# Performance work log

Hardware: AMD Instinct MI355X
Metric: run time of the kernel (lower is better)

The kernel has to match this reference:

```python
import jax, jax.numpy as jnp
import numpy as np

DIM = 512
HEADS = 8
DIM_HEAD = 64
INNER = HEADS * DIM_HEAD
SCALE = DIM_HEAD ** -0.5


def setup_inputs() -> dict:
    key = jax.random.key(0)
    ks = jax.random.split(key, 6)
    b, n = 2, 2048
    x = jax.random.normal(ks[0], (b, n, DIM), dtype=jnp.float32)
    # torch Linear(dim, 3*inner, bias=False): store as [in, out] for x @ W
    w_qkv = jax.random.normal(ks[1], (DIM, 3 * INNER), dtype=jnp.float32) * (DIM ** -0.5)
    # Conv2d(heads, heads, 1, bias=False) weights squeezed to [out_h, in_h]
    w_pre = jax.random.normal(ks[2], (HEADS, HEADS), dtype=jnp.float32) * (HEADS ** -0.5)
    w_post = jax.random.normal(ks[3], (HEADS, HEADS), dtype=jnp.float32) * (HEADS ** -0.5)
    w_out = jax.random.normal(ks[4], (INNER, DIM), dtype=jnp.float32) * (INNER ** -0.5)
    b_out = jax.random.normal(ks[5], (DIM,), dtype=jnp.float32) * 0.01
    return {"x": x, "w_qkv": w_qkv, "w_pre": w_pre, "w_post": w_post,
            "w_out": w_out, "b_out": b_out}


def reference(x, w_qkv, w_pre, w_post, w_out, b_out):
    b, n, _ = x.shape
    qkv = x @ w_qkv  # [b, n, 3*inner]
    q, k, v = jnp.split(qkv, 3, axis=-1)
    # b n (h d) -> b h n d
    split_heads = lambda t: t.reshape(b, n, HEADS, DIM_HEAD).transpose(0, 2, 1, 3)
    q, k, v = split_heads(q), split_heads(k), split_heads(v)
    dots = jnp.einsum('bhid,bhjd->bhij', q, k) * SCALE
    # pre-softmax talking-heads: 1x1 conv over the head axis
    dots = jnp.einsum('gh,bhij->bgij', w_pre, dots)
    attn = jax.nn.softmax(dots, axis=-1)
    # post-softmax talking-heads mix
    attn = jnp.einsum('gh,bhij->bgij', w_post, attn)
    out = jnp.einsum('bhij,bhjd->bhid', attn, v)
    out = out.transpose(0, 2, 1, 3).reshape(b, n, INNER)  # b h n d -> b n (h d)
    return out @ w_out + b_out
```

## Files before the change

kernel.cpp:

```cpp
#include <hip/hip_runtime.h>
#include <hip/hip_bf16.h>

typedef unsigned short ushort_t;
typedef __attribute__((ext_vector_type(8))) short short8;
typedef __attribute__((ext_vector_type(4))) short short4v;
typedef __attribute__((ext_vector_type(4))) float floatx4;

#define MFMA16(a, b, c) __builtin_amdgcn_mfma_f32_16x16x32_bf16(a, b, c, 0, 0, 0)

__device__ __forceinline__ float bf2f(ushort_t u) {
    unsigned int v = ((unsigned int)u) << 16;
    return __int_as_float((int)v);
}
__device__ __forceinline__ ushort_t f2bf(float f) {
    unsigned int x = (unsigned int)__float_as_int(f);
    unsigned int r = (x + 0x7FFFu + ((x >> 16) & 1u)) >> 16;
    return (ushort_t)r;
}
__device__ __forceinline__ floatx4 fma4(float a, floatx4 b, floatx4 c) {
    c[0] = fmaf(a, b[0], c[0]);
    c[1] = fmaf(a, b[1], c[1]);
    c[2] = fmaf(a, b[2], c[2]);
    c[3] = fmaf(a, b[3], c[3]);
    return c;
}

__global__ __launch_bounds__(256) void k_cvt(const floatx4* __restrict__ src,
                                             short4v* __restrict__ dst, int n4) {
    int i = blockIdx.x * 256 + threadIdx.x;
    if (i < n4) {
        floatx4 v = src[i];
        short4v o;
        o[0] = (short)f2bf(v[0]);
        o[1] = (short)f2bf(v[1]);
        o[2] = (short)f2bf(v[2]);
        o[3] = (short)f2bf(v[3]);
        dst[i] = o;
    }
}

__global__ __launch_bounds__(256) void k_transpose_cvt(const float* __restrict__ src,
                                                       ushort_t* __restrict__ dst, int R, int C) {
    __shared__ float t[32][33];
    int tx = threadIdx.x & 31, ty = threadIdx.x >> 5;
    int r0 = blockIdx.y * 32, c0 = blockIdx.x * 32;
    for (int y = ty; y < 32; y += 8) t[y][tx] = src[(r0 + y) * C + c0 + tx];
    __syncthreads();
    for (int y = ty; y < 32; y += 8) dst[(c0 + y) * R + r0 + tx] = f2bf(t[tx][y]);
}

__global__ __launch_bounds__(256) void k_qkv(const ushort_t* __restrict__ x,
                                             const ushort_t* __restrict__ wt,
                                             ushort_t* __restrict__ qs,
                                             ushort_t* __restrict__ ks,
                                             ushort_t* __restrict__ vt) {
    __shared__ __align__(16) ushort_t st[64 * 72];
    const int tid = threadIdx.x, lane = tid & 63, wv = tid >> 6;
    const int col = lane & 15, quad = lane >> 4;
    const int row0 = blockIdx.y * 64 + (wv >> 1) * 32;
    const int c0 = blockIdx.x * 64 + (wv & 1) * 32;
    const int which = blockIdx.x >> 3, hh = blockIdx.x & 7;
    const int brow0 = blockIdx.y * 64;
    const int bb = brow0 >> 11, n0 = brow0 & 2047;
    const int hidx = bb * 8 + hh;
    floatx4 acc[2][2];
#pragma unroll
    for (int i = 0; i < 2; i++)
#pragma unroll
        for (int j = 0; j < 2; j++) acc[i][j] = (floatx4){0.f, 0.f, 0.f, 0.f};
    for (int k0 = 0; k0 < 512; k0 += 32) {
        const int ko = k0 + quad * 8;
        short8 a0 = *(const short8*)&x[(row0 + col) * 512 + ko];
        short8 a1 = *(const short8*)&x[(row0 + 16 + col) * 512 + ko];
        short8 b0 = *(const short8*)&wt[(c0 + col) * 512 + ko];
        short8 b1 = *(const short8*)&wt[(c0 + 16 + col) * 512 + ko];
        acc[0][0] = MFMA16(a0, b0, acc[0][0]);
        acc[0][1] = MFMA16(a0, b1, acc[0][1]);
        acc[1][0] = MFMA16(a1, b0, acc[1][0]);
        acc[1][1] = MFMA16(a1, b1, acc[1][1]);
    }
    const float qscale = (which == 0) ? 0.125f : 1.0f;
#pragma unroll
    for (int i = 0; i < 2; i++)
#pragma unroll
        for (int j = 0; j < 2; j++)
#pragma unroll
            for (int r = 0; r < 4; r++) {
                int il = (wv >> 1) * 32 + i * 16 + quad * 4 + r;
                int cl = (wv & 1) * 32 + j * 16 + col;
                ushort_t hv = f2bf(acc[i][j][r] * qscale);
                if (which == 2) st[cl * 72 + il] = hv;
                else            st[il * 72 + cl] = hv;
            }
    __syncthreads();
    if (which < 2) {
        ushort_t* dst = (which == 0) ? qs : ks;
#pragma unroll
        for (int s = tid; s < 512; s += 256) {
            int rr = s >> 3, dc = (s & 7) * 8;
            *(short8*)&dst[(hidx * 2048 + n0 + rr) * 64 + dc] = *(const short8*)&st[rr * 72 + dc];
        }
    } else {
#pragma unroll
        for (int s = tid; s < 512; s += 256) {
            int d = s >> 3, nc = (s & 7) * 8;
            *(short8*)&vt[(hidx * 64 + d) * 2048 + n0 + nc] = *(const short8*)&st[d * 72 + nc];
        }
    }
}

__global__ __launch_bounds__(512, 2) void k_attn(const ushort_t* __restrict__ qs,
                                                 const ushort_t* __restrict__ ks,
                                                 const ushort_t* __restrict__ vt,
                                                 const float* __restrict__ w_pre,
                                                 const float* __restrict__ w_post,
                                                 const ushort_t* __restrict__ wot,
                                                 const float* __restrict__ bias,
                                                 float* __restrict__ out) {
    __shared__ __align__(16) ushort_t qlds[8 * 16 * 72];
    __shared__ __align__(16) ushort_t A[2][8 * 16 * 136];
    __shared__ __align__(16) ushort_t oline[16 * 520];
    __shared__ __align__(16) float wbuf[128];
    __shared__ float lred[8][8][16];
    __shared__ __align__(16) float linv[8][16];
    const int tid = threadIdx.x, lane = tid & 63, wv = tid >> 6;
    const int col = lane & 15, quad = lane >> 4;
    const int b = blockIdx.y, n0 = blockIdx.x * 16;
    const int e = wv;

    if (tid < 64) wbuf[tid] = w_pre[tid];
    else if (tid < 128) wbuf[tid] = w_post[tid - 64];
    for (int c = tid; c < 1024; c += 512) {
        int hh = c >> 7, rem = c & 127, ii = rem >> 3, dc = (rem & 7) * 8;
        *(short8*)&qlds[(hh * 16 + ii) * 72 + dc] =
            *(const short8*)&qs[((b * 8 + hh) * 2048 + n0 + ii) * 64 + dc];
    }

    short8 kb0[8], kb1[8];
#pragma unroll
    for (int h = 0; h < 8; h++) {
        const ushort_t* kp = &ks[((b * 8 + h) * 2048 + wv * 16 + col) * 64 + quad * 8];
        kb0[h] = *(const short8*)&kp[0];
        kb1[h] = *(const short8*)&kp[32];
    }
    __syncthreads();

    short8 qa0[8], qa1[8];
#pragma unroll
    for (int h = 0; h < 8; h++) {
        const ushort_t* qb = &qlds[(h * 16 + col) * 72 + quad * 8];
        qa0[h] = *(const short8*)&qb[0];
        qa1[h] = *(const short8*)&qb[32];
    }

    floatx4 Lacc[8];
#pragma unroll
    for (int g = 0; g < 8; g++) Lacc[g] = (floatx4){0.f, 0.f, 0.f, 0.f};

    for (int jt = 0; jt < 16; jt++) {
        floatx4 S[8];
#pragma unroll
        for (int h = 0; h < 8; h++) {
            floatx4 a = (floatx4){0.f, 0.f, 0.f, 0.f};
            a = MFMA16(qa0[h], kb0[h], a);
            a = MFMA16(qa1[h], kb1[h], a);
            S[h] = a;
        }
        if (jt < 15) {
            const int jw = (jt + 1) * 128 + wv * 16;
#pragma unroll
            for (int h = 0; h < 8; h++) {
                const ushort_t* kp = &ks[((b * 8 + h) * 2048 + jw + col) * 64 + quad * 8];
                kb0[h] = *(const short8*)&kp[0];
                kb1[h] = *(const short8*)&kp[32];
            }
        }
#pragma unroll
        for (int g = 0; g < 8; g++) {
            floatx4 w0 = *(const floatx4*)&wbuf[g * 8];
            floatx4 w1 = *(const floatx4*)&wbuf[g * 8 + 4];
            floatx4 s4 = (floatx4){0.f, 0.f, 0.f, 0.f};
#pragma unroll
            for (int h = 0; h < 4; h++) s4 = fma4(w0[h], S[h], s4);
#pragma unroll
            for (int h = 0; h < 4; h++) s4 = fma4(w1[h], S[h + 4], s4);
            floatx4 u4;
            u4[0] = __expf(s4[0]);
            u4[1] = __expf(s4[1]);
            u4[2] = __expf(s4[2]);
            u4[3] = __expf(s4[3]);
            Lacc[g] += u4;
        }
    }

#pragma unroll
    for (int g = 0; g < 8; g++)
#pragma unroll
        for (int r = 0; r < 4; r++) {
            float v = Lacc[g][r];
            v += __shfl_xor(v, 1, 64);
            v += __shfl_xor(v, 2, 64);
            v += __shfl_xor(v, 4, 64);
            v += __shfl_xor(v, 8, 64);
            if (col == 0) lred[wv][g][quad * 4 + r] = v;
        }
    __syncthreads();
    if (tid < 128) {
        int g = tid >> 4, ii = tid & 15;
        float l = 0.f;
#pragma unroll
        for (int w2 = 0; w2 < 8; w2++) l += lred[w2][g][ii];
        linv[g][ii] = 1.0f / l;
    }
    __syncthreads();

#pragma unroll
    for (int h = 0; h < 8; h++) {
        const ushort_t* kp = &ks[((b * 8 + h) * 2048 + wv * 16 + col) * 64 + quad * 8];
        kb0[h] = *(const short8*)&kp[0];
        kb1[h] = *(const short8*)&kp[32];
    }
    short8 vbr[16];
#pragma unroll
    for (int k2 = 0; k2 < 4; k2++)
#pragma unroll
        for (int nt = 0; nt < 4; nt++)
            vbr[k2 * 4 + nt] = *(const short8*)&vt[((b * 8 + e) * 64 + nt * 16 + col) * 2048 +
                                                   k2 * 32 + quad * 8];
    floatx4 Oa[4];
#pragma unroll
    for (int nt = 0; nt < 4; nt++) Oa[nt] = (floatx4){0.f, 0.f, 0.f, 0.f};

    int cur = 0;
    for (int jt = 0; jt < 16; jt++) {
        floatx4 S[8];
#pragma unroll
        for (int h = 0; h < 8; h++) {
            const ushort_t* qb = &qlds[(h * 16 + col) * 72 + quad * 8];
            short8 a0 = *(const short8*)&qb[0];
            short8 a1 = *(const short8*)&qb[32];
            floatx4 a = (floatx4){0.f, 0.f, 0.f, 0.f};
            a = MFMA16(a0, kb0[h], a);
            a = MFMA16(a1, kb1[h], a);
            S[h] = a;
        }
        if (jt < 15) {
            const int jw = (jt + 1) * 128 + wv * 16;
#pragma unroll
            for (int h = 0; h < 8; h++) {
                const ushort_t* kp = &ks[((b * 8 + h) * 2048 + jw + col) * 64 + quad * 8];
                kb0[h] = *(const short8*)&kp[0];
                kb1[h] = *(const short8*)&kp[32];
            }
        }
        floatx4 Ug[8];
#pragma unroll
        for (int g = 0; g < 8; g++) {
            floatx4 w0 = *(const floatx4*)&wbuf[g * 8];
            floatx4 w1 = *(const floatx4*)&wbuf[g * 8 + 4];
            floatx4 s4 = (floatx4){0.f, 0.f, 0.f, 0.f};
#pragma unroll
            for (int h = 0; h < 4; h++) s4 = fma4(w0[h], S[h], s4);
#pragma unroll
            for (int h = 0; h < 4; h++) s4 = fma4(w1[h], S[h + 4], s4);
            floatx4 lg = *(const floatx4*)&linv[g][quad * 4];
            floatx4 u4;
            u4[0] = __expf(s4[0]) * lg[0];
            u4[1] = __expf(s4[1]) * lg[1];
            u4[2] = __expf(s4[2]) * lg[2];
            u4[3] = __expf(s4[3]) * lg[3];
            Ug[g] = u4;
        }
        ushort_t* Ac = A[cur];
#pragma unroll
        for (int e2 = 0; e2 < 8; e2++) {
            floatx4 wqa = *(const floatx4*)&wbuf[64 + e2 * 8];
            floatx4 wqb = *(const floatx4*)&wbuf[64 + e2 * 8 + 4];
            floatx4 a4 = (floatx4){0.f, 0.f, 0.f, 0.f};
#pragma unroll
            for (int g = 0; g < 4; g++) a4 = fma4(wqa[g], Ug[g], a4);
#pragma unroll
            for (int g = 0; g < 4; g++) a4 = fma4(wqb[g], Ug[g + 4], a4);
#pragma unroll
            for (int r = 0; r < 4; r++)
                Ac[(e2 * 16 + quad * 4 + r) * 136 + wv * 16 + col] = f2bf(a4[r]);
        }
        asm volatile("s_waitcnt lgkmcnt(0)\n\ts_barrier" ::: "memory");
#pragma unroll
        for (int k2 = 0; k2 < 4; k2++) {
            short8 af = *(const short8*)&Ac[(e * 16 + col) * 136 + k2 * 32 + quad * 8];
#pragma unroll
            for (int nt = 0; nt < 4; nt++) Oa[nt] = MFMA16(af, vbr[k2 * 4 + nt], Oa[nt]);
        }
        if (jt < 15) {
            const int j0 = (jt + 1) * 128;
#pragma unroll
            for (int k2 = 0; k2 < 4; k2++)
#pragma unroll
                for (int nt = 0; nt < 4; nt++)
                    vbr[k2 * 4 + nt] =
                        *(const short8*)&vt[((b * 8 + e) * 64 + nt * 16 + col) * 2048 + j0 +
                                            k2 * 32 + quad * 8];
        }
        cur ^= 1;
    }

#pragma unroll
    for (int nt = 0; nt < 4; nt++)
#pragma unroll
        for (int r = 0; r < 4; r++)
            oline[(quad * 4 + r) * 520 + e * 64 + nt * 16 + col] = f2bf(Oa[nt][r]);
    __syncthreads();
#pragma unroll
    for (int nt = 0; nt < 4; nt++) {
        floatx4 acc = (floatx4){0.f, 0.f, 0.f, 0.f};
        const int c = wv * 64 + nt * 16 + col;
#pragma unroll
        for (int k2 = 0; k2 < 16; k2++) {
            short8 af = *(const short8*)&oline[col * 520 + k2 * 32 + quad * 8];
            short8 bf = *(const short8*)&wot[c * 512 + k2 * 32 + quad * 8];
            acc = MFMA16(af, bf, acc);
        }
        float bz = bias[c];
#pragma unroll
        for (int r = 0; r < 4; r++)
            out[(b * 2048 + n0 + quad * 4 + r) * 512 + c] = acc[r] + bz;
    }
}

extern "C" void kernel_launch(void* const* d_in, const int* in_sizes, int n_in,
                              void* d_out, int out_size, void* d_ws, size_t ws_size,
                              hipStream_t stream) {
    const float* x = (const float*)d_in[0];
    const float* w_qkv = (const float*)d_in[1];
    const float* w_pre = (const float*)d_in[2];
    const float* w_post = (const float*)d_in[3];
    const float* w_out = (const float*)d_in[4];
    const float* b_out = (const float*)d_in[5];
    char* ws = (char*)d_ws;
    ushort_t* qs = (ushort_t*)(ws);
    ushort_t* ks = (ushort_t*)(ws + (4u << 20));
    ushort_t* vt = (ushort_t*)(ws + (8u << 20));
    ushort_t* xb = (ushort_t*)(ws + (12u << 20));
    ushort_t* wt = (ushort_t*)(ws + (16u << 20));
    ushort_t* wot = (ushort_t*)(ws + (16u << 20) + 1572864u);
    float* out = (float*)d_out;

    k_cvt<<<dim3(2048), dim3(256), 0, stream>>>((const floatx4*)x, (short4v*)xb, 524288);
    k_transpose_cvt<<<dim3(48, 16), dim3(256), 0, stream>>>(w_qkv, wt, 512, 1536);
    k_transpose_cvt<<<dim3(16, 16), dim3(256), 0, stream>>>(w_out, wot, 512, 512);
    k_qkv<<<dim3(24, 64), dim3(256), 0, stream>>>(xb, wt, qs, ks, vt);
    k_attn<<<dim3(128, 2), dim3(512), 0, stream>>>(qs, ks, vt, w_pre, w_post, wot, b_out, out);
}
```

Before: 343.5 us.

## Split attention into row-sum, split-KV attention and projection kernels

The fused attention kernel is split into three kernels. A row-sum kernel computes partial softmax denominators over four key chunks. The attention kernel processes half the keys per block and writes fp32 partial outputs. A projection kernel sums the two halves and applies the output projection and bias. The old grid was only 256 blocks, and this split raises it to 512–1024 blocks to fill the GPU's compute units. In exchange it adds global round-trips for the partial sums and partial outputs, plus extra launches, and the A buffer loses its double buffering, which costs an extra barrier per iteration.

```diff
diff --git a/kernel.cpp b/kernel.cpp
--- a/kernel.cpp
+++ b/kernel.cpp
@@ -109,55 +109,39 @@
     }
 }
 
-__global__ __launch_bounds__(512, 2) void k_attn(const ushort_t* __restrict__ qs,
+__global__ __launch_bounds__(256, 4) void k_lsum(const ushort_t* __restrict__ qs,
                                                  const ushort_t* __restrict__ ks,
-                                                 const ushort_t* __restrict__ vt,
                                                  const float* __restrict__ w_pre,
-                                                 const float* __restrict__ w_post,
-                                                 const ushort_t* __restrict__ wot,
-                                                 const float* __restrict__ bias,
-                                                 float* __restrict__ out) {
-    __shared__ __align__(16) ushort_t qlds[8 * 16 * 72];
-    __shared__ __align__(16) ushort_t A[2][8 * 16 * 136];
-    __shared__ __align__(16) ushort_t oline[16 * 520];
-    __shared__ __align__(16) float wbuf[128];
-    __shared__ float lred[8][8][16];
-    __shared__ __align__(16) float linv[8][16];
+                                                 float* __restrict__ lpart) {
+    __shared__ float wpre_s[64];
+    __shared__ float lredL[4][8][16];
     const int tid = threadIdx.x, lane = tid & 63, wv = tid >> 6;
     const int col = lane & 15, quad = lane >> 4;
     const int b = blockIdx.y, n0 = blockIdx.x * 16;
-    const int e = wv;
-
-    if (tid < 64) wbuf[tid] = w_pre[tid];
-    else if (tid < 128) wbuf[tid] = w_post[tid - 64];
-    for (int c = tid; c < 1024; c += 512) {
-        int hh = c >> 7, rem = c & 127, ii = rem >> 3, dc = (rem & 7) * 8;
-        *(short8*)&qlds[(hh * 16 + ii) * 72 + dc] =
-            *(const short8*)&qs[((b * 8 + hh) * 2048 + n0 + ii) * 64 + dc];
-    }
-
-    short8 kb0[8], kb1[8];
+    const int jt = blockIdx.z * 4 + wv;
+    if (tid < 64) wpre_s[tid] = w_pre[tid];
+    __syncthreads();
+
+    short8 qa0[8], qa1[8];
 #pragma unroll
     for (int h = 0; h < 8; h++) {
-        const ushort_t* kp = &ks[((b * 8 + h) * 2048 + wv * 16 + col) * 64 + quad * 8];
-        kb0[h] = *(const short8*)&kp[0];
-        kb1[h] = *(const short8*)&kp[32];
-    }
-    __syncthreads();
-
-    short8 qa0[8], qa1[8];
-#pragma unroll
-    for (int h = 0; h < 8; h++) {
-        const ushort_t* qb = &qlds[(h * 16 + col) * 72 + quad * 8];
+        const ushort_t* qb = &qs[((b * 8 + h) * 2048 + n0 + col) * 64 + quad * 8];
         qa0[h] = *(const short8*)&qb[0];
         qa1[h] = *(const short8*)&qb[32];
     }
-
     floatx4 Lacc[8];
 #pragma unroll
     for (int g = 0; g < 8; g++) Lacc[g] = (floatx4){0.f, 0.f, 0.f, 0.f};
 
-    for (int jt = 0; jt < 16; jt++) {
+    for (int jc = 0; jc < 8; jc++) {
+        const int j0 = jt * 128 + jc * 16;
+        short8 kb0[8], kb1[8];
+#pragma unroll
+        for (int h = 0; h < 8; h++) {
+            const ushort_t* kp = &ks[((b * 8 + h) * 2048 + j0 + col) * 64 + quad * 8];
+            kb0[h] = *(const short8*)&kp[0];
+            kb1[h] = *(const short8*)&kp[32];
+        }
         floatx4 S[8];
 #pragma unroll
         for (int h = 0; h < 8; h++) {
@@ -166,19 +150,10 @@
             a = MFMA16(qa1[h], kb1[h], a);
             S[h] = a;
         }
-        if (jt < 15) {
-            const int jw = (jt + 1) * 128 + wv * 16;
-#pragma unroll
-            for (int h = 0; h < 8; h++) {
-                const ushort_t* kp = &ks[((b * 8 + h) * 2048 + jw + col) * 64 + quad * 8];
-                kb0[h] = *(const short8*)&kp[0];
-                kb1[h] = *(const short8*)&kp[32];
-            }
-        }
 #pragma unroll
         for (int g = 0; g < 8; g++) {
-            floatx4 w0 = *(const floatx4*)&wbuf[g * 8];
-            floatx4 w1 = *(const floatx4*)&wbuf[g * 8 + 4];
+            floatx4 w0 = *(const floatx4*)&wpre_s[g * 8];
+            floatx4 w1 = *(const floatx4*)&wpre_s[g * 8 + 4];
             floatx4 s4 = (floatx4){0.f, 0.f, 0.f, 0.f};
 #pragma unroll
             for (int h = 0; h < 4; h++) s4 = fma4(w0[h], S[h], s4);
@@ -192,7 +167,6 @@
             Lacc[g] += u4;
         }
     }
-
 #pragma unroll
     for (int g = 0; g < 8; g++)
 #pragma unroll
@@ -202,21 +176,52 @@
             v += __shfl_xor(v, 2, 64);
             v += __shfl_xor(v, 4, 64);
             v += __shfl_xor(v, 8, 64);
-            if (col == 0) lred[wv][g][quad * 4 + r] = v;
-        }
-    __syncthreads();
+            if (col == 0) lredL[wv][g][quad * 4 + r] = v;
+        }
+    __syncthreads();
+    if (tid < 128) {
+        int g = tid >> 4, ii = tid & 15;
+        float s = lredL[0][g][ii] + lredL[1][g][ii] + lredL[2][g][ii] + lredL[3][g][ii];
+        lpart[(blockIdx.z * 16 + b * 8 + g) * 2048 + n0 + ii] = s;
+    }
+}
+
+__global__ __launch_bounds__(512, 4) void k_attn(const ushort_t* __restrict__ qs,
+                                                 const ushort_t* __restrict__ ks,
+                                                 const ushort_t* __restrict__ vt,
+                                                 const float* __restrict__ w_pre,
+                                                 const float* __restrict__ w_post,
+                                                 const float* __restrict__ lpart,
+                                                 float* __restrict__ opart) {
+    __shared__ __align__(16) ushort_t qlds[8 * 16 * 72];
+    __shared__ __align__(16) ushort_t A[8 * 16 * 136];
+    __shared__ __align__(16) float wbuf[128];
+    __shared__ __align__(16) float linv_s[8][16];
+    const int tid = threadIdx.x, lane = tid & 63, wv = tid >> 6;
+    const int col = lane & 15, quad = lane >> 4;
+    const int b = blockIdx.y, n0 = blockIdx.x * 16;
+    const int jb = blockIdx.z * 8;
+    const int e = wv;
+
+    if (tid < 64) wbuf[tid] = w_pre[tid];
+    else if (tid < 128) wbuf[tid] = w_post[tid - 64];
     if (tid < 128) {
         int g = tid >> 4, ii = tid & 15;
         float l = 0.f;
 #pragma unroll
-        for (int w2 = 0; w2 < 8; w2++) l += lred[w2][g][ii];
-        linv[g][ii] = 1.0f / l;
-    }
-    __syncthreads();
-
+        for (int p = 0; p < 4; p++) l += lpart[(p * 16 + b * 8 + g) * 2048 + n0 + ii];
+        linv_s[g][ii] = 1.0f / l;
+    }
+    for (int c = tid; c < 1024; c += 512) {
+        int hh = c >> 7, rem = c & 127, ii = rem >> 3, dc = (rem & 7) * 8;
+        *(short8*)&qlds[(hh * 16 + ii) * 72 + dc] =
+            *(const short8*)&qs[((b * 8 + hh) * 2048 + n0 + ii) * 64 + dc];
+    }
+
+    short8 kb0[8], kb1[8];
 #pragma unroll
     for (int h = 0; h < 8; h++) {
-        const ushort_t* kp = &ks[((b * 8 + h) * 2048 + wv * 16 + col) * 64 + quad * 8];
+        const ushort_t* kp = &ks[((b * 8 + h) * 2048 + jb * 128 + wv * 16 + col) * 64 + quad * 8];
         kb0[h] = *(const short8*)&kp[0];
         kb1[h] = *(const short8*)&kp[32];
     }
@@ -226,13 +231,14 @@
 #pragma unroll
         for (int nt = 0; nt < 4; nt++)
             vbr[k2 * 4 + nt] = *(const short8*)&vt[((b * 8 + e) * 64 + nt * 16 + col) * 2048 +
-                                                   k2 * 32 + quad * 8];
+                                                   jb * 128 + k2 * 32 + quad * 8];
     floatx4 Oa[4];
 #pragma unroll
     for (int nt = 0; nt < 4; nt++) Oa[nt] = (floatx4){0.f, 0.f, 0.f, 0.f};
-
-    int cur = 0;
-    for (int jt = 0; jt < 16; jt++) {
+    __syncthreads();
+
+    for (int t = 0; t < 8; t++) {
+        const int jt = jb + t;
         floatx4 S[8];
 #pragma unroll
         for (int h = 0; h < 8; h++) {
@@ -244,7 +250,7 @@
             a = MFMA16(a1, kb1[h], a);
             S[h] = a;
         }
-        if (jt < 15) {
+        if (t < 7) {
             const int jw = (jt + 1) * 128 + wv * 16;
 #pragma unroll
             for (int h = 0; h < 8; h++) {
@@ -263,7 +269,7 @@
             for (int h = 0; h < 4; h++) s4 = fma4(w0[h], S[h], s4);
 #pragma unroll
             for (int h = 0; h < 4; h++) s4 = fma4(w1[h], S[h + 4], s4);
-            floatx4 lg = *(const floatx4*)&linv[g][quad * 4];
+            floatx4 lg = *(const floatx4*)&linv_s[g][quad * 4];
             floatx4 u4;
             u4[0] = __expf(s4[0]) * lg[0];
             u4[1] = __expf(s4[1]) * lg[1];
@@ -271,7 +277,7 @@
             u4[3] = __expf(s4[3]) * lg[3];
             Ug[g] = u4;
         }
-        ushort_t* Ac = A[cur];
+        asm volatile("s_waitcnt lgkmcnt(0)\n\ts_barrier" ::: "memory");
 #pragma unroll
         for (int e2 = 0; e2 < 8; e2++) {
             floatx4 wqa = *(const floatx4*)&wbuf[64 + e2 * 8];
@@ -283,16 +289,16 @@
             for (int g = 0; g < 4; g++) a4 = fma4(wqb[g], Ug[g + 4], a4);
 #pragma unroll
             for (int r = 0; r < 4; r++)
-                Ac[(e2 * 16 + quad * 4 + r) * 136 + wv * 16 + col] = f2bf(a4[r]);
+                A[(e2 * 16 + quad * 4 + r) * 136 + wv * 16 + col] = f2bf(a4[r]);
         }
         asm volatile("s_waitcnt lgkmcnt(0)\n\ts_barrier" ::: "memory");
 #pragma unroll
         for (int k2 = 0; k2 < 4; k2++) {
-            short8 af = *(const short8*)&Ac[(e * 16 + col) * 136 + k2 * 32 + quad * 8];
+            short8 af = *(const short8*)&A[(e * 16 + col) * 136 + k2 * 32 + quad * 8];
 #pragma unroll
             for (int nt = 0; nt < 4; nt++) Oa[nt] = MFMA16(af, vbr[k2 * 4 + nt], Oa[nt]);
         }
-        if (jt < 15) {
+        if (t < 7) {
             const int j0 = (jt + 1) * 128;
 #pragma unroll
             for (int k2 = 0; k2 < 4; k2++)
@@ -302,19 +308,43 @@
                         *(const short8*)&vt[((b * 8 + e) * 64 + nt * 16 + col) * 2048 + j0 +
                                             k2 * 32 + quad * 8];
         }
-        cur ^= 1;
     }
 
 #pragma unroll
     for (int nt = 0; nt < 4; nt++)
 #pragma unroll
         for (int r = 0; r < 4; r++)
-            oline[(quad * 4 + r) * 520 + e * 64 + nt * 16 + col] = f2bf(Oa[nt][r]);
-    __syncthreads();
-#pragma unroll
-    for (int nt = 0; nt < 4; nt++) {
+            opart[((blockIdx.z * 2 + b) * 2048 + n0 + quad * 4 + r) * 512 + e * 64 + nt * 16 +
+                  col] = Oa[nt][r];
+}
+
+__global__ __launch_bounds__(256) void k_proj(const float* __restrict__ opart,
+                                              const ushort_t* __restrict__ wot,
+                                              const float* __restrict__ bias,
+                                              float* __restrict__ out) {
+    __shared__ __align__(16) ushort_t oline[16 * 520];
+    const int tid = threadIdx.x, lane = tid & 63, wv = tid >> 6;
+    const int col = lane & 15, quad = lane >> 4;
+    const int b = blockIdx.y, n0 = blockIdx.x * 16;
+#pragma unroll
+    for (int it = 0; it < 8; it++) {
+        int idx = it * 256 + tid;
+        int row = idx >> 7, c4 = (idx & 127) << 2;
+        floatx4 v0 = *(const floatx4*)&opart[((0 + b) * 2048 + n0 + row) * 512 + c4];
+        floatx4 v1 = *(const floatx4*)&opart[((2 + b) * 2048 + n0 + row) * 512 + c4];
+        floatx4 s = v0 + v1;
+        short4v o;
+        o[0] = (short)f2bf(s[0]);
+        o[1] = (short)f2bf(s[1]);
+        o[2] = (short)f2bf(s[2]);
+        o[3] = (short)f2bf(s[3]);
+        *(short4v*)&oline[row * 520 + c4] = o;
+    }
+    __syncthreads();
+#pragma unroll
+    for (int ct = 0; ct < 4; ct++) {
         floatx4 acc = (floatx4){0.f, 0.f, 0.f, 0.f};
-        const int c = wv * 64 + nt * 16 + col;
+        const int c = blockIdx.z * 256 + wv * 64 + ct * 16 + col;
 #pragma unroll
         for (int k2 = 0; k2 < 16; k2++) {
             short8 af = *(const short8*)&oline[col * 520 + k2 * 32 + quad * 8];
@@ -344,11 +374,15 @@
     ushort_t* xb = (ushort_t*)(ws + (12u << 20));
     ushort_t* wt = (ushort_t*)(ws + (16u << 20));
     ushort_t* wot = (ushort_t*)(ws + (16u << 20) + 1572864u);
+    float* lpart = (float*)(ws + (18u << 20));
+    float* opart = (float*)(ws + (19u << 20));
     float* out = (float*)d_out;
 
     k_cvt<<<dim3(2048), dim3(256), 0, stream>>>((const floatx4*)x, (short4v*)xb, 524288);
     k_transpose_cvt<<<dim3(48, 16), dim3(256), 0, stream>>>(w_qkv, wt, 512, 1536);
     k_transpose_cvt<<<dim3(16, 16), dim3(256), 0, stream>>>(w_out, wot, 512, 512);
     k_qkv<<<dim3(24, 64), dim3(256), 0, stream>>>(xb, wt, qs, ks, vt);
-    k_attn<<<dim3(128, 2), dim3(512), 0, stream>>>(qs, ks, vt, w_pre, w_post, wot, b_out, out);
-}
+    k_lsum<<<dim3(128, 2, 4), dim3(256), 0, stream>>>(qs, ks, w_pre, lpart);
+    k_attn<<<dim3(128, 2, 2), dim3(512), 0, stream>>>(qs, ks, vt, w_pre, w_post, lpart, opart);
+    k_proj<<<dim3(128, 2, 2), dim3(256), 0, stream>>>(opart, wot, b_out, out);
+}
```

Result: slower. 593.1 us (+72.7%).
